# Kernel tuning notes

Measured on AMD Instinct MI355X. Metric: run time of the kernel, lower is better.

Reference implementation:

```python
import jax, jax.numpy as jnp
import numpy as np

LAYERS = 5      # lstm_layers
H = 1           # lstm_hidden_size
IN = 21         # 9 (rot) + 6 (v) + 6 (u)
NEG = 0.1       # LeakyReLU negative slope
EPS = 1e-5      # BatchNorm1d eps


def _lstm_cell(x, h, c, w_ih, w_hh):
    # torch gate order: i, f, g, o ; no biases (lstm_bias=False)
    gates = x @ w_ih.T + h @ w_hh.T              # [k, 4H]
    i, f, g, o = jnp.split(gates, 4, axis=-1)
    i = jax.nn.sigmoid(i)
    f = jax.nn.sigmoid(f)
    g = jnp.tanh(g)
    o = jax.nn.sigmoid(o)
    c_new = f * c + i * g
    h_new = o * jnp.tanh(c_new)
    return h_new, c_new


def _bn_train(z, gamma, beta):
    # BatchNorm1d in training mode: batch stats, biased variance
    m = z.mean(axis=0)
    var = z.var(axis=0)
    return gamma * (z - m) / jnp.sqrt(var + EPS) + beta


def setup_inputs() -> dict:
    key = jax.random.key(0)
    ks = jax.random.split(key, 14)
    k, T = 65536, 32
    s = 0.2  # init scale, roughly torch uniform(-1/sqrt(H)) magnitude
    inp = {
        "r": jax.random.normal(ks[0], (k, T, 9), jnp.float32),
        "v": jax.random.normal(ks[1], (k, T, 6), jnp.float32),
        "u": jax.random.normal(ks[2], (k, T, 6), jnp.float32),
        # LSTM weights: layer 0 sees IN features, layers 1..4 see H
        "w_ih0": jax.random.normal(ks[3], (4 * H, IN), jnp.float32) * s,
        "w_ih_rest": jax.random.normal(ks[4], (LAYERS - 1, 4 * H, H), jnp.float32) * s,
        "w_hh": jax.random.normal(ks[5], (LAYERS, 4 * H, H), jnp.float32) * s,
        # FC head: Linear(H,32,no bias) -> BN -> LReLU -> Linear(32,32) -> BN -> LReLU -> Linear(32,6)
        "W1": jax.random.normal(ks[6], (32, H), jnp.float32) * s,
        "g1": jnp.ones((32,), jnp.float32),
        "b1": jnp.zeros((32,), jnp.float32),
        "W2": jax.random.normal(ks[7], (32, 32), jnp.float32) * s,
        "g2": jnp.ones((32,), jnp.float32),
        "b2": jnp.zeros((32,), jnp.float32),
        "W3": jax.random.normal(ks[8], (6, 32), jnp.float32) * s,
    }
    return inp


def reference(r, v, u, w_ih0, w_ih_rest, w_hh, W1, g1, b1, W2, g2, b2, W3):
    x = jnp.concatenate([r, v, u], axis=-1)          # [k, T, 21]
    k = x.shape[0]
    h0 = jnp.zeros((LAYERS, k, H), x.dtype)
    c0 = jnp.zeros((LAYERS, k, H), x.dtype)
    xs = jnp.swapaxes(x, 0, 1)                       # [T, k, 21]

    def step(carry, xt):
        h, c = carry
        hs, cs = [], []
        layer_in = xt
        for l in range(LAYERS):
            w_ih = w_ih0 if l == 0 else w_ih_rest[l - 1]
            hl, cl = _lstm_cell(layer_in, h[l], c[l], w_ih, w_hh[l])
            hs.append(hl)
            cs.append(cl)
            layer_in = hl
        return (jnp.stack(hs), jnp.stack(cs)), layer_in  # top-layer output

    (hT, cT), outs = jax.lax.scan(step, (h0, c0), xs)    # outs: [T, k, H]

    # fc applied to out[:, 0] -> first timestep of top layer
    y = outs[0]                                          # [k, H]
    y = jax.nn.leaky_relu(_bn_train(y @ W1.T, g1, b1), NEG)
    y = jax.nn.leaky_relu(_bn_train(y @ W2.T, g2, b2), NEG)
    dv = y @ W3.T                                        # [k, 6]
    return dv[:, None], hT, cT
```

## Files before the change

### kernel.cpp

```cpp
#include <hip/hip_runtime.h>
#include <math.h>

#define T 32
#define NEGS 0.1f
#define EPS 1e-5f

__device__ __forceinline__ float sigm(float x) {
    return 1.0f / (1.0f + __expf(-x));
}
__device__ __forceinline__ float tanh_fast(float x) {
    float ax = fabsf(x);
    float t = __expf(2.0f * ax);
    float r = 1.0f - 2.0f / (t + 1.0f);
    return copysignf(r, x);
}
__device__ __forceinline__ float lrelu(float x) {
    return x > 0.0f ? x : NEGS * x;
}

__global__ __launch_bounds__(256, 1)
void lstm_kernel(const float* __restrict__ r, const float* __restrict__ v,
                 const float* __restrict__ u,
                 const float* __restrict__ wih0, const float* __restrict__ wihr,
                 const float* __restrict__ whhp,
                 float* __restrict__ out, double* __restrict__ wsd,
                 float* __restrict__ wsy, int k)
{
    const int s = blockIdx.x * 256 + threadIdx.x;

    float wi0[4][21];
#pragma unroll
    for (int g = 0; g < 4; ++g)
#pragma unroll
        for (int j = 0; j < 21; ++j) wi0[g][j] = wih0[g * 21 + j];
    float wir[4][4];
#pragma unroll
    for (int l = 0; l < 4; ++l)
#pragma unroll
        for (int g = 0; g < 4; ++g) wir[l][g] = wihr[l * 4 + g];
    float whh[5][4];
#pragma unroll
    for (int l = 0; l < 5; ++l)
#pragma unroll
        for (int g = 0; g < 4; ++g) whh[l][g] = whhp[l * 4 + g];

    const float4* r4 = reinterpret_cast<const float4*>(r + (size_t)s * (T * 9));
    const float4* v4 = reinterpret_cast<const float4*>(v + (size_t)s * (T * 6));
    const float4* u4 = reinterpret_cast<const float4*>(u + (size_t)s * (T * 6));

    float h[5] = {0.f, 0.f, 0.f, 0.f, 0.f};
    float c[5] = {0.f, 0.f, 0.f, 0.f, 0.f};
    float y0 = 0.f;

    for (int t0 = 0; t0 < T; t0 += 4) {
        const int cb = t0 >> 2;
        float4 rb[9], vb[6], ub[6];
#pragma unroll
        for (int q = 0; q < 9; ++q) rb[q] = r4[cb * 9 + q];
#pragma unroll
        for (int q = 0; q < 6; ++q) vb[q] = v4[cb * 6 + q];
#pragma unroll
        for (int q = 0; q < 6; ++q) ub[q] = u4[cb * 6 + q];

        float rf[36], vf[24], uf[24];
#pragma unroll
        for (int q = 0; q < 9; ++q) {
            rf[4 * q] = rb[q].x; rf[4 * q + 1] = rb[q].y;
            rf[4 * q + 2] = rb[q].z; rf[4 * q + 3] = rb[q].w;
        }
#pragma unroll
        for (int q = 0; q < 6; ++q) {
            vf[4 * q] = vb[q].x; vf[4 * q + 1] = vb[q].y;
            vf[4 * q + 2] = vb[q].z; vf[4 * q + 3] = vb[q].w;
            uf[4 * q] = ub[q].x; uf[4 * q + 1] = ub[q].y;
            uf[4 * q + 2] = ub[q].z; uf[4 * q + 3] = ub[q].w;
        }

#pragma unroll
        for (int dt = 0; dt < 4; ++dt) {
            float x[21];
#pragma unroll
            for (int j = 0; j < 9; ++j) x[j] = rf[dt * 9 + j];
#pragma unroll
            for (int j = 0; j < 6; ++j) x[9 + j] = vf[dt * 6 + j];
#pragma unroll
            for (int j = 0; j < 6; ++j) x[15 + j] = uf[dt * 6 + j];

            float gt[4];
#pragma unroll
            for (int g = 0; g < 4; ++g) {
                float a = whh[0][g] * h[0];
#pragma unroll
                for (int j = 0; j < 21; ++j) a = fmaf(wi0[g][j], x[j], a);
                gt[g] = a;
            }
            {
                float ii = sigm(gt[0]), ff = sigm(gt[1]);
                float gg = tanh_fast(gt[2]), oo = sigm(gt[3]);
                c[0] = ff * c[0] + ii * gg;
                h[0] = oo * tanh_fast(c[0]);
            }
            float xin = h[0];
#pragma unroll
            for (int l = 1; l < 5; ++l) {
                float g0 = fmaf(wir[l - 1][0], xin, whh[l][0] * h[l]);
                float g1 = fmaf(wir[l - 1][1], xin, whh[l][1] * h[l]);
                float g2 = fmaf(wir[l - 1][2], xin, whh[l][2] * h[l]);
                float g3 = fmaf(wir[l - 1][3], xin, whh[l][3] * h[l]);
                float ii = sigm(g0), ff = sigm(g1);
                float gg = tanh_fast(g2), oo = sigm(g3);
                c[l] = ff * c[l] + ii * gg;
                h[l] = oo * tanh_fast(c[l]);
                xin = h[l];
            }
            if (t0 + dt == 0) y0 = h[4];
        }
    }

#pragma unroll
    for (int l = 0; l < 5; ++l) {
        out[(size_t)6 * k + (size_t)l * k + s] = h[l];
        out[(size_t)11 * k + (size_t)l * k + s] = c[l];
    }
    wsy[s] = y0;

    float ys = y0, yq = y0 * y0;
#pragma unroll
    for (int off = 32; off; off >>= 1) {
        ys += __shfl_down(ys, off);
        yq += __shfl_down(yq, off);
    }
    __shared__ float pS[4], pQ[4];
    const int wid = threadIdx.x >> 6, lane = threadIdx.x & 63;
    if (lane == 0) { pS[wid] = ys; pQ[wid] = yq; }
    __syncthreads();
    if (threadIdx.x == 0) {
        atomicAdd(&wsd[0], (double)(pS[0] + pS[1] + pS[2] + pS[3]));
        atomicAdd(&wsd[1], (double)(pQ[0] + pQ[1] + pQ[2] + pQ[3]));
    }
}

__global__ __launch_bounds__(256)
void fc_stats_kernel(const float* __restrict__ W1, const float* __restrict__ g1v,
                     const float* __restrict__ b1v, const float* __restrict__ W2,
                     double* __restrict__ wsd, const float* __restrict__ wsy, int k)
{
    __shared__ float sW2[1024];
    __shared__ float sA[32], sBv[32];
    __shared__ float sMy;
    for (int i = threadIdx.x; i < 1024; i += 256) sW2[i] = W2[i];
    if (threadIdx.x < 32) {
        float my = (float)(wsd[0] / k);
        float vy = (float)(wsd[1] / k) - my * my;
        int j = threadIdx.x;
        float wj = W1[j];
        sA[j] = g1v[j] * wj * rsqrtf(fmaf(wj * wj, vy, EPS));
        sBv[j] = b1v[j];
        if (j == 0) sMy = my;
    }
    __syncthreads();

    const int s = blockIdx.x * 256 + threadIdx.x;
    const float yc = wsy[s] - sMy;
    float y1[32];
#pragma unroll
    for (int j = 0; j < 32; ++j) y1[j] = lrelu(fmaf(sA[j], yc, sBv[j]));

    __shared__ float pS[4][32], pQ[4][32];
    const int wid = threadIdx.x >> 6, lane = threadIdx.x & 63;
    for (int i = 0; i < 32; ++i) {
        float z = 0.f;
#pragma unroll
        for (int j = 0; j < 32; ++j) z = fmaf(sW2[i * 32 + j], y1[j], z);
        float q = z * z;
#pragma unroll
        for (int off = 32; off; off >>= 1) {
            z += __shfl_down(z, off);
            q += __shfl_down(q, off);
        }
        if (lane == 0) { pS[wid][i] = z; pQ[wid][i] = q; }
    }
    __syncthreads();
    if (threadIdx.x < 32) {
        int i = threadIdx.x;
        atomicAdd(&wsd[2 + i], (double)(pS[0][i] + pS[1][i] + pS[2][i] + pS[3][i]));
    } else if (threadIdx.x < 64) {
        int i = threadIdx.x - 32;
        atomicAdd(&wsd[34 + i], (double)(pQ[0][i] + pQ[1][i] + pQ[2][i] + pQ[3][i]));
    }
}

__global__ __launch_bounds__(256)
void fc_final_kernel(const float* __restrict__ W1, const float* __restrict__ g1v,
                     const float* __restrict__ b1v, const float* __restrict__ W2,
                     const float* __restrict__ g2v, const float* __restrict__ b2v,
                     const float* __restrict__ W3, const double* __restrict__ wsd,
                     const float* __restrict__ wsy, float* __restrict__ out, int k)
{
    __shared__ float sW2[1024], sW3[192];
    __shared__ float sA[32], sBv[32], sM2[32], sI2[32], sB2[32];
    __shared__ float sMy;
    for (int i = threadIdx.x; i < 1024; i += 256) sW2[i] = W2[i];
    if (threadIdx.x < 192) sW3[threadIdx.x] = W3[threadIdx.x];
    if (threadIdx.x < 32) {
        float my = (float)(wsd[0] / k);
        float vy = (float)(wsd[1] / k) - my * my;
        int j = threadIdx.x;
        float wj = W1[j];
        sA[j] = g1v[j] * wj * rsqrtf(fmaf(wj * wj, vy, EPS));
        sBv[j] = b1v[j];
        float m2 = (float)(wsd[2 + j] / k);
        float v2 = (float)(wsd[34 + j] / k) - m2 * m2;
        sM2[j] = m2;
        sI2[j] = g2v[j] * rsqrtf(v2 + EPS);
        sB2[j] = b2v[j];
        if (j == 0) sMy = my;
    }
    __syncthreads();

    const int s = blockIdx.x * 256 + threadIdx.x;
    const float yc = wsy[s] - sMy;
    float y1[32];
#pragma unroll
    for (int j = 0; j < 32; ++j) y1[j] = lrelu(fmaf(sA[j], yc, sBv[j]));

    float dv[6] = {0.f, 0.f, 0.f, 0.f, 0.f, 0.f};
    for (int i = 0; i < 32; ++i) {
        float z = 0.f;
#pragma unroll
        for (int j = 0; j < 32; ++j) z = fmaf(sW2[i * 32 + j], y1[j], z);
        float y2 = lrelu(fmaf(sI2[i], z - sM2[i], sB2[i]));
#pragma unroll
        for (int m = 0; m < 6; ++m) dv[m] = fmaf(sW3[m * 32 + i], y2, dv[m]);
    }
#pragma unroll
    for (int m = 0; m < 6; ++m) out[(size_t)s * 6 + m] = dv[m];
}

extern "C" void kernel_launch(void* const* d_in, const int* in_sizes, int n_in,
                              void* d_out, int out_size, void* d_ws, size_t ws_size,
                              hipStream_t stream)
{
    const float* r    = (const float*)d_in[0];
    const float* v    = (const float*)d_in[1];
    const float* u    = (const float*)d_in[2];
    const float* wih0 = (const float*)d_in[3];
    const float* wihr = (const float*)d_in[4];
    const float* whhp = (const float*)d_in[5];
    const float* W1   = (const float*)d_in[6];
    const float* g1v  = (const float*)d_in[7];
    const float* b1v  = (const float*)d_in[8];
    const float* W2   = (const float*)d_in[9];
    const float* g2v  = (const float*)d_in[10];
    const float* b2v  = (const float*)d_in[11];
    const float* W3   = (const float*)d_in[12];

    const int k = in_sizes[0] / (T * 9);
    float* out = (float*)d_out;
    double* wsd = (double*)d_ws;
    float* wsy = (float*)((char*)d_ws + 1024);

    hipMemsetAsync(d_ws, 0, 1024, stream);

    const int blocks = k / 256;
    lstm_kernel<<<blocks, 256, 0, stream>>>(r, v, u, wih0, wihr, whhp, out, wsd, wsy, k);
    fc_stats_kernel<<<blocks, 256, 0, stream>>>(W1, g1v, b1v, W2, wsd, wsy, k);
    fc_final_kernel<<<blocks, 256, 0, stream>>>(W1, g1v, b1v, W2, g2v, b2v, W3, wsd, wsy, out, k);
}
```

Measured before the change: 267.1 us.

## Replace FC stats pass with piecewise-linear region histogram and precomputed tables

Because H=1, each first-layer unit after LeakyReLU is piecewise linear in the scalar y, so samples are binned into 33 regions by the sorted BN1 thresholds. Per-region count, sum and sum of squares are histogrammed, and the second BatchNorm's statistics are computed analytically in a single-block tables kernel. That kernel also emits per-region affine coefficients, so the final kernel skips the 32x32 matmul. Separately, the LSTM kernel now precomputes the input projections for each 4-step chunk and prefetches the next chunk, and uses hardware reciprocal for sigmoid and tanh. The costs are an extra serial single-block launch, float shared-memory atomics that may contend on hot bins, float accumulation of large sums, and lower-precision reciprocal.

After: 366.0 us. +37.0%, slower.

```diff
diff --git a/kernel.cpp b/kernel.cpp
--- a/kernel.cpp
+++ b/kernel.cpp
@@ -4,18 +4,36 @@
 #define T 32
 #define NEGS 0.1f
 #define EPS 1e-5f
-
-__device__ __forceinline__ float sigm(float x) {
-    return 1.0f / (1.0f + __expf(-x));
-}
+#define NREG 33
+
+
+__device__ __forceinline__ float rcp_fast(float x) { return __builtin_amdgcn_rcpf(x); }
+__device__ __forceinline__ float sigm(float x) { return rcp_fast(1.0f + __expf(-x)); }
 __device__ __forceinline__ float tanh_fast(float x) {
-    float ax = fabsf(x);
-    float t = __expf(2.0f * ax);
-    float r = 1.0f - 2.0f / (t + 1.0f);
+    float t = __expf(2.0f * fabsf(x));
+    float r = 1.0f - 2.0f * rcp_fast(t + 1.0f);
     return copysignf(r, x);
 }
-__device__ __forceinline__ float lrelu(float x) {
-    return x > 0.0f ? x : NEGS * x;
+__device__ __forceinline__ float lrelu(float x) { return x > 0.0f ? x : NEGS * x; }
+__device__ __forceinline__ float f4c(const float4 f, int c) {
+    switch (c & 3) { case 0: return f.x; case 1: return f.y; case 2: return f.z; default: return f.w; }
+}
+
+__device__ __forceinline__ void bn1_params(const float* __restrict__ W1,
+                                           const float* __restrict__ g1,
+                                           const float* __restrict__ b1,
+                                           const double* __restrict__ wsd, int k, int j,
+                                           float& my, float& vy, float& a, float& b,
+                                           float& tau, int& flip)
+{
+    my = (float)(wsd[0] / k);
+    vy = (float)(wsd[1] / k) - my * my;
+    float wj = W1[j];
+    a = g1[j] * wj * rsqrtf(fmaf(wj * wj, vy, EPS));
+    b = b1[j];
+    if (a > 0.0f)      { tau = my - b / a; flip = 0; }
+    else if (a < 0.0f) { tau = my - b / a; flip = 1; }
+    else               { tau = (b > 0.0f ? -__builtin_inff() : __builtin_inff()); flip = 0; }
 }
 
 __global__ __launch_bounds__(256, 1)
@@ -48,72 +66,69 @@
     const float4* v4 = reinterpret_cast<const float4*>(v + (size_t)s * (T * 6));
     const float4* u4 = reinterpret_cast<const float4*>(u + (size_t)s * (T * 6));
 
+    float4 rb[9], vb[6], ub[6];
+#pragma unroll
+    for (int q = 0; q < 9; ++q) rb[q] = r4[q];
+#pragma unroll
+    for (int q = 0; q < 6; ++q) vb[q] = v4[q];
+#pragma unroll
+    for (int q = 0; q < 6; ++q) ub[q] = u4[q];
+
     float h[5] = {0.f, 0.f, 0.f, 0.f, 0.f};
     float c[5] = {0.f, 0.f, 0.f, 0.f, 0.f};
     float y0 = 0.f;
 
-    for (int t0 = 0; t0 < T; t0 += 4) {
-        const int cb = t0 >> 2;
-        float4 rb[9], vb[6], ub[6];
-#pragma unroll
-        for (int q = 0; q < 9; ++q) rb[q] = r4[cb * 9 + q];
-#pragma unroll
-        for (int q = 0; q < 6; ++q) vb[q] = v4[cb * 6 + q];
-#pragma unroll
-        for (int q = 0; q < 6; ++q) ub[q] = u4[cb * 6 + q];
-
-        float rf[36], vf[24], uf[24];
-#pragma unroll
-        for (int q = 0; q < 9; ++q) {
-            rf[4 * q] = rb[q].x; rf[4 * q + 1] = rb[q].y;
-            rf[4 * q + 2] = rb[q].z; rf[4 * q + 3] = rb[q].w;
-        }
-#pragma unroll
-        for (int q = 0; q < 6; ++q) {
-            vf[4 * q] = vb[q].x; vf[4 * q + 1] = vb[q].y;
-            vf[4 * q + 2] = vb[q].z; vf[4 * q + 3] = vb[q].w;
-            uf[4 * q] = ub[q].x; uf[4 * q + 1] = ub[q].y;
-            uf[4 * q + 2] = ub[q].z; uf[4 * q + 3] = ub[q].w;
-        }
-
+#pragma unroll
+    for (int cb = 0; cb < 8; ++cb) {
+        float xg[4][4];
 #pragma unroll
         for (int dt = 0; dt < 4; ++dt) {
-            float x[21];
-#pragma unroll
-            for (int j = 0; j < 9; ++j) x[j] = rf[dt * 9 + j];
-#pragma unroll
-            for (int j = 0; j < 6; ++j) x[9 + j] = vf[dt * 6 + j];
-#pragma unroll
-            for (int j = 0; j < 6; ++j) x[15 + j] = uf[dt * 6 + j];
-
-            float gt[4];
 #pragma unroll
             for (int g = 0; g < 4; ++g) {
-                float a = whh[0][g] * h[0];
-#pragma unroll
-                for (int j = 0; j < 21; ++j) a = fmaf(wi0[g][j], x[j], a);
-                gt[g] = a;
+                float acc = 0.f;
+#pragma unroll
+                for (int j = 0; j < 9; ++j) acc = fmaf(wi0[g][j], f4c(rb[(dt * 9 + j) >> 2], dt * 9 + j), acc);
+#pragma unroll
+                for (int j = 0; j < 6; ++j) acc = fmaf(wi0[g][9 + j], f4c(vb[(dt * 6 + j) >> 2], dt * 6 + j), acc);
+#pragma unroll
+                for (int j = 0; j < 6; ++j) acc = fmaf(wi0[g][15 + j], f4c(ub[(dt * 6 + j) >> 2], dt * 6 + j), acc);
+                xg[dt][g] = acc;
             }
+        }
+        if (cb < 7) {
+#pragma unroll
+            for (int q = 0; q < 9; ++q) rb[q] = r4[(cb + 1) * 9 + q];
+#pragma unroll
+            for (int q = 0; q < 6; ++q) vb[q] = v4[(cb + 1) * 6 + q];
+#pragma unroll
+            for (int q = 0; q < 6; ++q) ub[q] = u4[(cb + 1) * 6 + q];
+        }
+#pragma unroll
+        for (int dt = 0; dt < 4; ++dt) {
+            float g0 = fmaf(whh[0][0], h[0], xg[dt][0]);
+            float g1 = fmaf(whh[0][1], h[0], xg[dt][1]);
+            float g2 = fmaf(whh[0][2], h[0], xg[dt][2]);
+            float g3 = fmaf(whh[0][3], h[0], xg[dt][3]);
             {
-                float ii = sigm(gt[0]), ff = sigm(gt[1]);
-                float gg = tanh_fast(gt[2]), oo = sigm(gt[3]);
+                float ii = sigm(g0), ff = sigm(g1);
+                float gg = tanh_fast(g2), oo = sigm(g3);
                 c[0] = ff * c[0] + ii * gg;
                 h[0] = oo * tanh_fast(c[0]);
             }
             float xin = h[0];
 #pragma unroll
             for (int l = 1; l < 5; ++l) {
-                float g0 = fmaf(wir[l - 1][0], xin, whh[l][0] * h[l]);
-                float g1 = fmaf(wir[l - 1][1], xin, whh[l][1] * h[l]);
-                float g2 = fmaf(wir[l - 1][2], xin, whh[l][2] * h[l]);
-                float g3 = fmaf(wir[l - 1][3], xin, whh[l][3] * h[l]);
-                float ii = sigm(g0), ff = sigm(g1);
-                float gg = tanh_fast(g2), oo = sigm(g3);
+                float a0 = fmaf(wir[l - 1][0], xin, whh[l][0] * h[l]);
+                float a1 = fmaf(wir[l - 1][1], xin, whh[l][1] * h[l]);
+                float a2 = fmaf(wir[l - 1][2], xin, whh[l][2] * h[l]);
+                float a3 = fmaf(wir[l - 1][3], xin, whh[l][3] * h[l]);
+                float ii = sigm(a0), ff = sigm(a1);
+                float gg = tanh_fast(a2), oo = sigm(a3);
                 c[l] = ff * c[l] + ii * gg;
                 h[l] = oo * tanh_fast(c[l]);
                 xin = h[l];
             }
-            if (t0 + dt == 0) y0 = h[4];
+            if (cb == 0 && dt == 0) y0 = h[4];
         }
     }
 
@@ -141,95 +156,162 @@
 }
 
 __global__ __launch_bounds__(256)
-void fc_stats_kernel(const float* __restrict__ W1, const float* __restrict__ g1v,
-                     const float* __restrict__ b1v, const float* __restrict__ W2,
-                     double* __restrict__ wsd, const float* __restrict__ wsy, int k)
-{
+void hist_kernel(const float* __restrict__ W1, const float* __restrict__ g1,
+                 const float* __restrict__ b1, double* __restrict__ wsd,
+                 const float* __restrict__ wsy, int k)
+{
+    __shared__ float sTau[32];
+    __shared__ float sH[3 * NREG];
+    __shared__ float sMy;
+    const int tid = threadIdx.x;
+    if (tid < 3 * NREG) sH[tid] = 0.f;
+    if (tid < 32) {
+        float my, vy, a, b, tau; int flip;
+        bn1_params(W1, g1, b1, wsd, k, tid, my, vy, a, b, tau, flip);
+        sTau[tid] = tau;
+        if (tid == 0) sMy = my;
+    }
+    __syncthreads();
+    const int s = blockIdx.x * 256 + tid;
+    const float y = wsy[s];
+    const float yc = y - sMy;
+    int rgn = 0;
+#pragma unroll
+    for (int j = 0; j < 32; ++j) rgn += (y > sTau[j]) ? 1 : 0;
+    atomicAdd(&sH[rgn], 1.0f);
+    atomicAdd(&sH[NREG + rgn], yc);
+    atomicAdd(&sH[2 * NREG + rgn], yc * yc);
+    __syncthreads();
+    if (tid < 3 * NREG) atomicAdd(&wsd[2 + tid], (double)sH[tid]);
+}
+
+__global__ __launch_bounds__(256)
+void tables_kernel(const float* __restrict__ W1, const float* __restrict__ g1,
+                   const float* __restrict__ b1, const float* __restrict__ W2,
+                   const float* __restrict__ g2, const float* __restrict__ b2,
+                   const double* __restrict__ wsd, float* __restrict__ gPQ, int k)
+{
+    __shared__ float sA[32], sB[32], sTau[32];
+    __shared__ int sRank[32], sFlip[32];
+    __shared__ float sS0[NREG], sS1[NREG], sS2[NREG];
     __shared__ float sW2[1024];
-    __shared__ float sA[32], sBv[32];
-    __shared__ float sMy;
-    for (int i = threadIdx.x; i < 1024; i += 256) sW2[i] = W2[i];
-    if (threadIdx.x < 32) {
-        float my = (float)(wsd[0] / k);
-        float vy = (float)(wsd[1] / k) - my * my;
-        int j = threadIdx.x;
-        float wj = W1[j];
-        sA[j] = g1v[j] * wj * rsqrtf(fmaf(wj * wj, vy, EPS));
-        sBv[j] = b1v[j];
-        if (j == 0) sMy = my;
-    }
-    __syncthreads();
-
-    const int s = blockIdx.x * 256 + threadIdx.x;
-    const float yc = wsy[s] - sMy;
-    float y1[32];
-#pragma unroll
-    for (int j = 0; j < 32; ++j) y1[j] = lrelu(fmaf(sA[j], yc, sBv[j]));
-
-    __shared__ float pS[4][32], pQ[4][32];
-    const int wid = threadIdx.x >> 6, lane = threadIdx.x & 63;
+    __shared__ float sSumY1[32];
+    __shared__ float sM[1024];
+    __shared__ float sI2[32], sM2v[32], sB2[32];
+    const int tid = threadIdx.x;
+
+    for (int i = tid; i < 1024; i += 256) sW2[i] = W2[i];
+    if (tid < NREG) {
+        sS0[tid] = (float)wsd[2 + tid];
+        sS1[tid] = (float)wsd[2 + NREG + tid];
+        sS2[tid] = (float)wsd[2 + 2 * NREG + tid];
+    }
+    if (tid < 32) {
+        float my, vy, a, b, tau; int flip;
+        bn1_params(W1, g1, b1, wsd, k, tid, my, vy, a, b, tau, flip);
+        sA[tid] = a; sB[tid] = b; sTau[tid] = tau; sFlip[tid] = flip;
+        sB2[tid] = b2[tid];
+    }
+    __syncthreads();
+    if (tid < 32) {
+        int rk = 0;
+        float tj = sTau[tid];
+#pragma unroll
+        for (int l = 0; l < 32; ++l)
+            rk += (sTau[l] < tj || (sTau[l] == tj && l < tid)) ? 1 : 0;
+        sRank[tid] = rk;
+    }
+    __syncthreads();
+    if (tid < 32) {
+        const int rk = sRank[tid], fl = sFlip[tid];
+        const float a = sA[tid], b = sB[tid];
+        float acc = 0.f;
+        for (int rg = 0; rg < NREG; ++rg) {
+            float m = (((rk < rg) ? 1 : 0) != fl) ? 1.0f : NEGS;
+            acc += m * (a * sS1[rg] + b * sS0[rg]);
+        }
+        sSumY1[tid] = acc;
+    }
+    for (int p = tid; p < 1024; p += 256) {
+        const int j = p >> 5, l = p & 31;
+        const int rj = sRank[j], fj = sFlip[j];
+        const int rl = sRank[l], flp = sFlip[l];
+        const float aj = sA[j], bj = sB[j], al = sA[l], bl = sB[l];
+        const float caa = aj * al, cab = aj * bl + al * bj, cbb = bj * bl;
+        float acc = 0.f;
+        for (int rg = 0; rg < NREG; ++rg) {
+            float mj = (((rj < rg) ? 1 : 0) != fj) ? 1.0f : NEGS;
+            float ml = (((rl < rg) ? 1 : 0) != flp) ? 1.0f : NEGS;
+            acc += mj * ml * (caa * sS2[rg] + cab * sS1[rg] + cbb * sS0[rg]);
+        }
+        sM[p] = acc;
+    }
+    __syncthreads();
+    if (tid < 32) {
+        const int i = tid;
+        float s2 = 0.f, ss2 = 0.f;
+#pragma unroll
+        for (int j = 0; j < 32; ++j) {
+            float wij = sW2[i * 32 + j];
+            s2 = fmaf(wij, sSumY1[j], s2);
+            float tj = 0.f;
+#pragma unroll
+            for (int l = 0; l < 32; ++l) tj = fmaf(sW2[i * 32 + l], sM[j * 32 + l], tj);
+            ss2 = fmaf(wij, tj, ss2);
+        }
+        float m2 = s2 / k;
+        float v2 = ss2 / k - m2 * m2;
+        sM2v[i] = m2;
+        sI2[i] = g2[i] * rsqrtf(v2 + EPS);
+    }
+    __syncthreads();
+    for (int idx = tid; idx < NREG * 32; idx += 256) {
+        const int rg = idx >> 5, i = idx & 31;
+        float Ai = 0.f, Bi = 0.f;
+#pragma unroll
+        for (int j = 0; j < 32; ++j) {
+            float m = (((sRank[j] < rg) ? 1 : 0) != sFlip[j]) ? 1.0f : NEGS;
+            float w = sW2[i * 32 + j] * m;
+            Ai = fmaf(w, sA[j], Ai);
+            Bi = fmaf(w, sB[j], Bi);
+        }
+        gPQ[idx] = sI2[i] * Ai;
+        gPQ[NREG * 32 + idx] = sI2[i] * (Bi - sM2v[i]) + sB2[i];
+    }
+}
+
+__global__ __launch_bounds__(256)
+void final_kernel(const float* __restrict__ W1, const float* __restrict__ g1,
+                  const float* __restrict__ b1, const float* __restrict__ W3,
+                  const double* __restrict__ wsd, const float* __restrict__ wsy,
+                  const float* __restrict__ gPQ, float* __restrict__ out, int k)
+{
+    __shared__ float sTau[32], sW3[192], sMy;
+    __shared__ float sP[NREG][33], sQ[NREG][33];
+    const int tid = threadIdx.x;
+    for (int idx = tid; idx < NREG * 32; idx += 256) {
+        const int rg = idx >> 5, i = idx & 31;
+        sP[rg][i] = gPQ[idx];
+        sQ[rg][i] = gPQ[NREG * 32 + idx];
+    }
+    if (tid < 192) sW3[tid] = W3[tid];
+    if (tid < 32) {
+        float my, vy, a, b, tau; int flip;
+        bn1_params(W1, g1, b1, wsd, k, tid, my, vy, a, b, tau, flip);
+        sTau[tid] = tau;
+        if (tid == 0) sMy = my;
+    }
+    __syncthreads();
+    const int s = blockIdx.x * 256 + tid;
+    const float y = wsy[s];
+    const float yc = y - sMy;
+    int rgn = 0;
+#pragma unroll
+    for (int j = 0; j < 32; ++j) rgn += (y > sTau[j]) ? 1 : 0;
+    float dv[6] = {0.f, 0.f, 0.f, 0.f, 0.f, 0.f};
+#pragma unroll
     for (int i = 0; i < 32; ++i) {
-        float z = 0.f;
-#pragma unroll
-        for (int j = 0; j < 32; ++j) z = fmaf(sW2[i * 32 + j], y1[j], z);
-        float q = z * z;
-#pragma unroll
-        for (int off = 32; off; off >>= 1) {
-            z += __shfl_down(z, off);
-            q += __shfl_down(q, off);
-        }
-        if (lane == 0) { pS[wid][i] = z; pQ[wid][i] = q; }
-    }
-    __syncthreads();
-    if (threadIdx.x < 32) {
-        int i = threadIdx.x;
-        atomicAdd(&wsd[2 + i], (double)(pS[0][i] + pS[1][i] + pS[2][i] + pS[3][i]));
-    } else if (threadIdx.x < 64) {
-        int i = threadIdx.x - 32;
-        atomicAdd(&wsd[34 + i], (double)(pQ[0][i] + pQ[1][i] + pQ[2][i] + pQ[3][i]));
-    }
-}
-
-__global__ __launch_bounds__(256)
-void fc_final_kernel(const float* __restrict__ W1, const float* __restrict__ g1v,
-                     const float* __restrict__ b1v, const float* __restrict__ W2,
-                     const float* __restrict__ g2v, const float* __restrict__ b2v,
-                     const float* __restrict__ W3, const double* __restrict__ wsd,
-                     const float* __restrict__ wsy, float* __restrict__ out, int k)
-{
-    __shared__ float sW2[1024], sW3[192];
-    __shared__ float sA[32], sBv[32], sM2[32], sI2[32], sB2[32];
-    __shared__ float sMy;
-    for (int i = threadIdx.x; i < 1024; i += 256) sW2[i] = W2[i];
-    if (threadIdx.x < 192) sW3[threadIdx.x] = W3[threadIdx.x];
-    if (threadIdx.x < 32) {
-        float my = (float)(wsd[0] / k);
-        float vy = (float)(wsd[1] / k) - my * my;
-        int j = threadIdx.x;
-        float wj = W1[j];
-        sA[j] = g1v[j] * wj * rsqrtf(fmaf(wj * wj, vy, EPS));
-        sBv[j] = b1v[j];
-        float m2 = (float)(wsd[2 + j] / k);
-        float v2 = (float)(wsd[34 + j] / k) - m2 * m2;
-        sM2[j] = m2;
-        sI2[j] = g2v[j] * rsqrtf(v2 + EPS);
-        sB2[j] = b2v[j];
-        if (j == 0) sMy = my;
-    }
-    __syncthreads();
-
-    const int s = blockIdx.x * 256 + threadIdx.x;
-    const float yc = wsy[s] - sMy;
-    float y1[32];
-#pragma unroll
-    for (int j = 0; j < 32; ++j) y1[j] = lrelu(fmaf(sA[j], yc, sBv[j]));
-
-    float dv[6] = {0.f, 0.f, 0.f, 0.f, 0.f, 0.f};
-    for (int i = 0; i < 32; ++i) {
-        float z = 0.f;
-#pragma unroll
-        for (int j = 0; j < 32; ++j) z = fmaf(sW2[i * 32 + j], y1[j], z);
-        float y2 = lrelu(fmaf(sI2[i], z - sM2[i], sB2[i]));
+        float y2 = lrelu(fmaf(sP[rgn][i], yc, sQ[rgn][i]));
 #pragma unroll
         for (int m = 0; m < 6; ++m) dv[m] = fmaf(sW3[m * 32 + i], y2, dv[m]);
     }
@@ -259,11 +341,13 @@
     float* out = (float*)d_out;
     double* wsd = (double*)d_ws;
     float* wsy = (float*)((char*)d_ws + 1024);
+    float* gPQ = (float*)((char*)d_ws + 1024 + (size_t)k * 4);
 
     hipMemsetAsync(d_ws, 0, 1024, stream);
 
     const int blocks = k / 256;
     lstm_kernel<<<blocks, 256, 0, stream>>>(r, v, u, wih0, wihr, whhp, out, wsd, wsy, k);
-    fc_stats_kernel<<<blocks, 256, 0, stream>>>(W1, g1v, b1v, W2, wsd, wsy, k);
-    fc_final_kernel<<<blocks, 256, 0, stream>>>(W1, g1v, b1v, W2, g2v, b2v, W3, wsd, wsy, out, k);
-}
+    hist_kernel<<<blocks, 256, 0, stream>>>(W1, g1v, b1v, wsd, wsy, k);
+    tables_kernel<<<1, 256, 0, stream>>>(W1, g1v, b1v, W2, g2v, b2v, wsd, gPQ, k);
+    final_kernel<<<blocks, 256, 0, stream>>>(W1, g1v, b1v, W3, wsd, wsy, gPQ, out, k);
+}
```
